# Kernel optimization log

Hardware: AMD Instinct MI355X
Metric: run time of the kernel (lower is better)

## Reference

```python
import jax, jax.numpy as jnp
import numpy as np

B, N, RBF, F = 4, 512, 32, 16
EPS = 1e-7


def _levi_civita():
    e = np.zeros((3, 3, 3), np.float32)
    e[0, 1, 2] = e[1, 2, 0] = e[2, 0, 1] = 1.0
    e[0, 2, 1] = e[2, 1, 0] = e[1, 0, 2] = -1.0
    return jnp.asarray(e)


def setup_inputs() -> dict:
    key = jax.random.key(0)
    ks = jax.random.split(key, 8)
    g = lambda k, s, sc=1.0: jax.random.normal(k, s, dtype=jnp.float32) * sc
    w_sc = RBF ** -0.5
    return dict(
        image=jax.random.uniform(ks[0], (B, N, N, RBF), dtype=jnp.float32),
        vectors=g(ks[1], (B, N, N, 3)),
        feat0=g(ks[2], (B, N, F, 1)),
        feat1=g(ks[3], (B, N, F, 3)),
        W00=g(ks[4], (RBF, F), w_sc), b00=jnp.zeros((F,), jnp.float32),
        W01=g(ks[5], (RBF, F), w_sc), b01=jnp.zeros((F,), jnp.float32),
        W10=g(ks[6], (RBF, F), w_sc), b10=jnp.zeros((F,), jnp.float32),
        W11=g(ks[7], (RBF, F), w_sc), b11=jnp.zeros((F,), jnp.float32),
    )


def _masked(radial, vectors):
    # zero the radial where the pair vector has (near) zero norm (self-pairs)
    keep = jnp.linalg.norm(vectors, axis=-1) >= EPS  # (B,N,N)
    return jnp.where(keep[..., None], radial, jnp.zeros_like(radial))


def reference(image, vectors, feat0, feat1, W00, b00, W01, b01, W10, b10, W11, b11):
    # radial networks: Dense(rbf -> F), one per (input tensor, filter order)
    r00 = image @ W00 + b00                      # (B,N,N,F) RO0 filter for RO0 input
    r01 = _masked(image @ W01 + b01, vectors)    # RO1 filter for RO0 input
    r10 = image @ W10 + b10                      # RO0 filter for RO1 input
    r11 = _masked(image @ W11 + b11, vectors)    # RO1 filter for RO1 input

    f0 = feat0[..., 0]                           # (B,N,F)
    # Note: RO1 filter F1[m,a,b,f,j] = vectors[m,a,b,j] * masked_radial[m,a,b,f];
    # fused into the einsums to avoid materializing (B,N,N,F,3).
    out1 = jnp.einsum('mabf,mbf->maf', r00, f0)[..., None]                 # 0x0->0
    out2 = jnp.einsum('mabi,mabf,mbf->mafi', vectors, r01, f0)             # 1x0->1
    out3 = jnp.einsum('mabf,mbfi->mafi', r10, feat1)                       # 0x1->1
    out4 = jnp.einsum('mabj,mabf,mbfj->maf', vectors, r11, feat1)[..., None]  # 1x1->0
    e = _levi_civita()
    out5 = jnp.einsum('ijk,mabj,mabf,mbfk->mafi', e, vectors, r11, feat1)  # 1x1->1
    return (out1, out2, out3, out4, out5)
```

## Files before the change

kernel.cpp:

```cpp
#include <hip/hip_runtime.h>
#include <hip/hip_bf16.h>


typedef __attribute__((ext_vector_type(8))) short short8;
typedef __attribute__((ext_vector_type(4))) float f32x4;

#define EPS2 1e-14f

static __device__ __forceinline__ short f2bf(float x) {
    __hip_bfloat16 h = __float2bfloat16(x);
    return *reinterpret_cast<short*>(&h);
}

__global__ __launch_bounds__(256, 4) void conv_mfma_vec_kernel(
    const float* __restrict__ image,
    const float* __restrict__ vectors,
    const float* __restrict__ feat0,
    const float* __restrict__ feat1,
    const float* __restrict__ W00, const float* __restrict__ b00,
    const float* __restrict__ W01, const float* __restrict__ b01,
    const float* __restrict__ W10, const float* __restrict__ b10,
    const float* __restrict__ W11, const float* __restrict__ b11,
    float* __restrict__ out)
{
    __shared__ float red[4][16][12];

    const int t    = threadIdx.x;
    const int wave = t >> 6;
    const int lane = t & 63;
    const int f    = lane & 15;
    const int g    = lane >> 4;
    const int ma   = blockIdx.x;
    const int m    = ma >> 9;

    short8 wf0, wf1, wf2, wf3;
    float bias0, bias1, bias2, bias3;
    {
        #pragma unroll
        for (int j = 0; j < 8; ++j) {
            const int k = g * 8 + j;
            wf0[j] = f2bf(W00[k * 16 + f]);
            wf1[j] = f2bf(W01[k * 16 + f]);
            wf2[j] = f2bf(W10[k * 16 + f]);
            wf3[j] = f2bf(W11[k * 16 + f]);
        }
        bias0 = b00[f]; bias1 = b01[f]; bias2 = b10[f]; bias3 = b11[f];
    }

    const float* imgbase = image   + (size_t)ma * (512 * 32);
    const float* vecbase = vectors + (size_t)ma * (512 * 3);
    const float* f0base  = feat0   + (size_t)m  * (512 * 16);
    const float* f1base  = feat1   + (size_t)m  * (512 * 16 * 3);

    float acc1 = 0.f, acc4 = 0.f;
    float acc2x = 0.f, acc2y = 0.f, acc2z = 0.f;
    float acc3x = 0.f, acc3y = 0.f, acc3z = 0.f;
    float acc5x = 0.f, acc5y = 0.f, acc5z = 0.f;

    const int bbase = wave * 128;

#define TAIL(R00, R01, R10, R11, VX, VY, VZ, F0V, U0, U1, U2) { \
    const float vx_ = (VX), vy_ = (VY), vz_ = (VZ); \
    const float n2_ = vx_ * vx_ + vy_ * vy_ + vz_ * vz_; \
    const bool keep_ = n2_ >= EPS2; \
    const float r00_ = (R00); \
    const float r01_ = keep_ ? (R01) : 0.f; \
    const float r10_ = (R10); \
    const float r11_ = keep_ ? (R11) : 0.f; \
    const float f0v_ = (F0V); \
    const float u0_ = (U0), u1_ = (U1), u2_ = (U2); \
    acc1 = fmaf(r00_, f0v_, acc1); \
    const float t01_ = r01_ * f0v_; \
    acc2x = fmaf(t01_, vx_, acc2x); \
    acc2y = fmaf(t01_, vy_, acc2y); \
    acc2z = fmaf(t01_, vz_, acc2z); \
    acc3x = fmaf(r10_, u0_, acc3x); \
    acc3y = fmaf(r10_, u1_, acc3y); \
    acc3z = fmaf(r10_, u2_, acc3z); \
    const float dd_ = fmaf(vx_, u0_, fmaf(vy_, u1_, vz_ * u2_)); \
    acc4 = fmaf(r11_, dd_, acc4); \
    acc5x = fmaf(r11_, vy_ * u2_ - vz_ * u1_, acc5x); \
    acc5y = fmaf(r11_, vz_ * u0_ - vx_ * u2_, acc5y); \
    acc5z = fmaf(r11_, vx_ * u1_ - vy_ * u0_, acc5z); \
}

    for (int tt = 0; tt < 8; ++tt) {
        const int b0 = bbase + tt * 16;

        const float* arow = imgbase + (size_t)(b0 + f) * 32 + g * 8;
        const float4 a0 = *(const float4*)(arow);
        const float4 a1 = *(const float4*)(arow + 4);

        const int bb = b0 + 4 * g;
        const float* vp = vecbase + bb * 3;
        const float4 V0 = *(const float4*)(vp);
        const float4 V1 = *(const float4*)(vp + 4);
        const float4 V2 = *(const float4*)(vp + 8);
        const float* f0p = f0base + bb * 16 + f;
        const float F0a = f0p[0], F0b = f0p[16], F0c = f0p[32], F0d = f0p[48];
        const float* f1p = f1base + (size_t)(bb * 16 + f) * 3;
        const float3 U_0 = *(const float3*)(f1p);
        const float3 U_1 = *(const float3*)(f1p + 48);
        const float3 U_2 = *(const float3*)(f1p + 96);
        const float3 U_3 = *(const float3*)(f1p + 144);

        short8 af;
        af[0] = f2bf(a0.x); af[1] = f2bf(a0.y);
        af[2] = f2bf(a0.z); af[3] = f2bf(a0.w);
        af[4] = f2bf(a1.x); af[5] = f2bf(a1.y);
        af[6] = f2bf(a1.z); af[7] = f2bf(a1.w);

        f32x4 d0 = {bias0, bias0, bias0, bias0};
        f32x4 d1 = {bias1, bias1, bias1, bias1};
        f32x4 d2 = {bias2, bias2, bias2, bias2};
        f32x4 d3 = {bias3, bias3, bias3, bias3};
        d0 = __builtin_amdgcn_mfma_f32_16x16x32_bf16(af, wf0, d0, 0, 0, 0);
        d1 = __builtin_amdgcn_mfma_f32_16x16x32_bf16(af, wf1, d1, 0, 0, 0);
        d2 = __builtin_amdgcn_mfma_f32_16x16x32_bf16(af, wf2, d2, 0, 0, 0);
        d3 = __builtin_amdgcn_mfma_f32_16x16x32_bf16(af, wf3, d3, 0, 0, 0);

        TAIL(d0[0], d1[0], d2[0], d3[0], V0.x, V0.y, V0.z, F0a, U_0.x, U_0.y, U_0.z)
        TAIL(d0[1], d1[1], d2[1], d3[1], V0.w, V1.x, V1.y, F0b, U_1.x, U_1.y, U_1.z)
        TAIL(d0[2], d1[2], d2[2], d3[2], V1.z, V1.w, V2.x, F0c, U_2.x, U_2.y, U_2.z)
        TAIL(d0[3], d1[3], d2[3], d3[3], V2.y, V2.z, V2.w, F0d, U_3.x, U_3.y, U_3.z)
    }
#undef TAIL

    #define WRED(x) x += __shfl_xor(x, 16); x += __shfl_xor(x, 32);
    WRED(acc1)  WRED(acc2x) WRED(acc2y) WRED(acc2z)
    WRED(acc3x) WRED(acc3y) WRED(acc3z) WRED(acc4)
    WRED(acc5x) WRED(acc5y) WRED(acc5z)
    #undef WRED

    if (lane < 16) {
        red[wave][f][0]  = acc1;
        red[wave][f][1]  = acc2x;
        red[wave][f][2]  = acc2y;
        red[wave][f][3]  = acc2z;
        red[wave][f][4]  = acc3x;
        red[wave][f][5]  = acc3y;
        red[wave][f][6]  = acc3z;
        red[wave][f][7]  = acc4;
        red[wave][f][8]  = acc5x;
        red[wave][f][9]  = acc5y;
        red[wave][f][10] = acc5z;
    }
    __syncthreads();

    if (t < 176) {
        const int ff = t / 11;
        const int comp = t % 11;
        float s = red[0][ff][comp] + red[1][ff][comp]
                + red[2][ff][comp] + red[3][ff][comp];

        const size_t base16 = (size_t)ma * 16 + ff;
        const size_t base48 = base16 * 3;
        if (comp == 0)      out[base16] = s;
        else if (comp < 4)  out[32768  + base48 + (comp - 1)] = s;
        else if (comp < 7)  out[131072 + base48 + (comp - 4)] = s;
        else if (comp == 7) out[229376 + base16] = s;
        else                out[262144 + base48 + (comp - 8)] = s;
    }
}

extern "C" void kernel_launch(void* const* d_in, const int* in_sizes, int n_in,
                              void* d_out, int out_size, void* d_ws, size_t ws_size,
                              hipStream_t stream) {
    const float* image   = (const float*)d_in[0];
    const float* vectors = (const float*)d_in[1];
    const float* feat0   = (const float*)d_in[2];
    const float* feat1   = (const float*)d_in[3];
    const float* W00 = (const float*)d_in[4];
    const float* b00 = (const float*)d_in[5];
    const float* W01 = (const float*)d_in[6];
    const float* b01 = (const float*)d_in[7];
    const float* W10 = (const float*)d_in[8];
    const float* b10 = (const float*)d_in[9];
    const float* W11 = (const float*)d_in[10];
    const float* b11 = (const float*)d_in[11];
    float* out = (float*)d_out;

    conv_mfma_vec_kernel<<<4 * 512, 256, 0, stream>>>(
        image, vectors, feat0, feat1,
        W00, b00, W01, b01, W10, b10, W11, b11, out);
}
```

Measured before the change: 226.0 us.

## Double-buffer image and feature tiles in LDS via async global_load_lds

Each wave now stages its image, feat0 and feat1 tiles into a per-wave double buffer in LDS using direct global-to-LDS loads. The next tile is prefetched while the current one is processed, and an XOR swizzle on image rows is meant to avoid bank conflicts. This aims to hide global load latency behind the MFMA and tail arithmetic. In exchange it uses about 48KB of LDS per block, lowers launch bounds occupancy from 4 to 3, and waits on vmcnt(0), which also stalls on the vector loads each iteration.

```diff
diff --git a/kernel.cpp b/kernel.cpp
--- a/kernel.cpp
+++ b/kernel.cpp
@@ -12,7 +12,14 @@
     return *reinterpret_cast<short*>(&h);
 }
 
-__global__ __launch_bounds__(256, 4) void conv_mfma_vec_kernel(
+static __device__ __forceinline__ void gload16(const void* g, void* l) {
+    __builtin_amdgcn_global_load_lds(
+        (const __attribute__((address_space(1))) void*)g,
+        (__attribute__((address_space(3))) void*)l,
+        16, 0, 0);
+}
+
+__global__ __launch_bounds__(256, 3) void conv_mfma_ldspipe_kernel(
     const float* __restrict__ image,
     const float* __restrict__ vectors,
     const float* __restrict__ feat0,
@@ -23,6 +30,7 @@
     const float* __restrict__ W11, const float* __restrict__ b11,
     float* __restrict__ out)
 {
+    __shared__ __align__(16) char smem[4 * 2 * 6144];
     __shared__ float red[4][16][12];
 
     const int t    = threadIdx.x;
@@ -58,6 +66,21 @@
     float acc5x = 0.f, acc5y = 0.f, acc5z = 0.f;
 
     const int bbase = wave * 128;
+    const unsigned wlds = (unsigned)wave * 12288u;
+
+#define STAGE(TT, DST) { \
+    const char* imgT_ = (const char*)(imgbase + (size_t)(bbase + (TT) * 16) * 32); \
+    const char* f0T_  = (const char*)(f0base + (bbase + (TT) * 16) * 16); \
+    const char* f1T_  = (const char*)(f1base + (size_t)(bbase + (TT) * 16) * 48); \
+    { const int i_ = lane;      const int r_ = i_ >> 3, s_ = i_ & 7; \
+      gload16(imgT_ + (((r_ << 3) + (s_ ^ (r_ & 7))) << 4), smem + (DST)); } \
+    { const int i_ = lane + 64; const int r_ = i_ >> 3, s_ = i_ & 7; \
+      gload16(imgT_ + (((r_ << 3) + (s_ ^ (r_ & 7))) << 4), smem + (DST) + 1024); } \
+    gload16(f0T_ + (lane << 4),        smem + (DST) + 2048); \
+    gload16(f1T_ + (lane << 4),        smem + (DST) + 3072); \
+    gload16(f1T_ + (lane << 4) + 1024, smem + (DST) + 4096); \
+    gload16(f1T_ + (lane << 4) + 2048, smem + (DST) + 5120); \
+}
 
 #define TAIL(R00, R01, R10, R11, VX, VY, VZ, F0V, U0, U1, U2) { \
     const float vx_ = (VX), vy_ = (VY), vz_ = (VZ); \
@@ -84,25 +107,46 @@
     acc5z = fmaf(r11_, vx_ * u1_ - vy_ * u0_, acc5z); \
 }
 
+    STAGE(0, wlds)
+
+    #pragma unroll
     for (int tt = 0; tt < 8; ++tt) {
-        const int b0 = bbase + tt * 16;
-
-        const float* arow = imgbase + (size_t)(b0 + f) * 32 + g * 8;
-        const float4 a0 = *(const float4*)(arow);
-        const float4 a1 = *(const float4*)(arow + 4);
-
-        const int bb = b0 + 4 * g;
+        const int cur = tt & 1;
+
+        asm volatile("s_waitcnt vmcnt(0)" ::: "memory");
+        __builtin_amdgcn_sched_barrier(0);
+
+        const char* cb = smem + wlds + (unsigned)cur * 6144u;
+        const float4 a0 = *(const float4*)(cb + f * 128 + (((2 * g)     ^ (f & 7)) << 4));
+        const float4 a1 = *(const float4*)(cb + f * 128 + (((2 * g + 1) ^ (f & 7)) << 4));
+        const float* f0s = (const float*)(cb + 2048);
+        const float F0a = f0s[(4 * g + 0) * 16 + f];
+        const float F0b = f0s[(4 * g + 1) * 16 + f];
+        const float F0c = f0s[(4 * g + 2) * 16 + f];
+        const float F0d = f0s[(4 * g + 3) * 16 + f];
+        const float* f1s = (const float*)(cb + 3072);
+        const float U00 = f1s[(4 * g + 0) * 48 + f * 3 + 0];
+        const float U01 = f1s[(4 * g + 0) * 48 + f * 3 + 1];
+        const float U02 = f1s[(4 * g + 0) * 48 + f * 3 + 2];
+        const float U10 = f1s[(4 * g + 1) * 48 + f * 3 + 0];
+        const float U11 = f1s[(4 * g + 1) * 48 + f * 3 + 1];
+        const float U12 = f1s[(4 * g + 1) * 48 + f * 3 + 2];
+        const float U20 = f1s[(4 * g + 2) * 48 + f * 3 + 0];
+        const float U21 = f1s[(4 * g + 2) * 48 + f * 3 + 1];
+        const float U22 = f1s[(4 * g + 2) * 48 + f * 3 + 2];
+        const float U30 = f1s[(4 * g + 3) * 48 + f * 3 + 0];
+        const float U31 = f1s[(4 * g + 3) * 48 + f * 3 + 1];
+        const float U32 = f1s[(4 * g + 3) * 48 + f * 3 + 2];
+
+        const int bb = bbase + tt * 16 + 4 * g;
         const float* vp = vecbase + bb * 3;
         const float4 V0 = *(const float4*)(vp);
         const float4 V1 = *(const float4*)(vp + 4);
         const float4 V2 = *(const float4*)(vp + 8);
-        const float* f0p = f0base + bb * 16 + f;
-        const float F0a = f0p[0], F0b = f0p[16], F0c = f0p[32], F0d = f0p[48];
-        const float* f1p = f1base + (size_t)(bb * 16 + f) * 3;
-        const float3 U_0 = *(const float3*)(f1p);
-        const float3 U_1 = *(const float3*)(f1p + 48);
-        const float3 U_2 = *(const float3*)(f1p + 96);
-        const float3 U_3 = *(const float3*)(f1p + 144);
+
+        __builtin_amdgcn_sched_barrier(0);
+        if (tt < 7) { STAGE(tt + 1, wlds + (unsigned)(cur ^ 1) * 6144u) }
+        __builtin_amdgcn_sched_barrier(0);
 
         short8 af;
         af[0] = f2bf(a0.x); af[1] = f2bf(a0.y);
@@ -119,12 +163,13 @@
         d2 = __builtin_amdgcn_mfma_f32_16x16x32_bf16(af, wf2, d2, 0, 0, 0);
         d3 = __builtin_amdgcn_mfma_f32_16x16x32_bf16(af, wf3, d3, 0, 0, 0);
 
-        TAIL(d0[0], d1[0], d2[0], d3[0], V0.x, V0.y, V0.z, F0a, U_0.x, U_0.y, U_0.z)
-        TAIL(d0[1], d1[1], d2[1], d3[1], V0.w, V1.x, V1.y, F0b, U_1.x, U_1.y, U_1.z)
-        TAIL(d0[2], d1[2], d2[2], d3[2], V1.z, V1.w, V2.x, F0c, U_2.x, U_2.y, U_2.z)
-        TAIL(d0[3], d1[3], d2[3], d3[3], V2.y, V2.z, V2.w, F0d, U_3.x, U_3.y, U_3.z)
+        TAIL(d0[0], d1[0], d2[0], d3[0], V0.x, V0.y, V0.z, F0a, U00, U01, U02)
+        TAIL(d0[1], d1[1], d2[1], d3[1], V0.w, V1.x, V1.y, F0b, U10, U11, U12)
+        TAIL(d0[2], d1[2], d2[2], d3[2], V1.z, V1.w, V2.x, F0c, U20, U21, U22)
+        TAIL(d0[3], d1[3], d2[3], d3[3], V2.y, V2.z, V2.w, F0d, U30, U31, U32)
     }
 #undef TAIL
+#undef STAGE
 
     #define WRED(x) x += __shfl_xor(x, 16); x += __shfl_xor(x, 32);
     WRED(acc1)  WRED(acc2x) WRED(acc2y) WRED(acc2z)
@@ -180,7 +225,7 @@
     const float* b11 = (const float*)d_in[11];
     float* out = (float*)d_out;
 
-    conv_mfma_vec_kernel<<<4 * 512, 256, 0, stream>>>(
+    conv_mfma_ldspipe_kernel<<<4 * 512, 256, 0, stream>>>(
         image, vectors, feat0, feat1,
         W00, b00, W01, b01, W10, b10, W11, b11, out);
 }
```

Measured after the change: 361.7 us. +60.1%, slower.

## Double-buffer image and feature tiles in LDS via async global-to-LDS loads

Applied to the files above, without the earlier changes.

Each wave now stages its image rows plus feat0 and feat1 slices into a per-wave double buffer in shared memory using global_load_lds. The next tile is prefetched while the current one is consumed. The image tile is stored with an XOR swizzle and a row permutation, so the MFMA output rows map to interleaved b indices, and the vector loads are remapped to match. The aim is to hide global-load latency in a kernel that is bandwidth- and latency-limited. The cost is 48KB of LDS per block, which may lower occupancy, and a block-wide barrier on every iteration.

```diff
diff --git a/kernel.cpp b/kernel.cpp
--- a/kernel.cpp
+++ b/kernel.cpp
@@ -12,7 +12,14 @@
     return *reinterpret_cast<short*>(&h);
 }
 
-__global__ __launch_bounds__(256, 4) void conv_mfma_vec_kernel(
+static __device__ __forceinline__ void gload16(const void* g, void* l) {
+    __builtin_amdgcn_global_load_lds(
+        (const __attribute__((address_space(1))) void*)g,
+        (__attribute__((address_space(3))) void*)l,
+        16, 0, 0);
+}
+
+__global__ __launch_bounds__(256, 4) void conv_mfma_coop_kernel(
     const float* __restrict__ image,
     const float* __restrict__ vectors,
     const float* __restrict__ feat0,
@@ -23,6 +30,7 @@
     const float* __restrict__ W11, const float* __restrict__ b11,
     float* __restrict__ out)
 {
+    __shared__ __align__(16) char smem[4 * 2 * 6144];
     __shared__ float red[4][16][12];
 
     const int t    = threadIdx.x;
@@ -58,6 +66,27 @@
     float acc5x = 0.f, acc5y = 0.f, acc5z = 0.f;
 
     const int bbase = wave * 128;
+    const unsigned wlds = (unsigned)wave * 12288u;
+
+    const int r0 = lane >> 3, s0 = lane & 7;
+    const int sr0 = ((r0 & 3) << 2) + (r0 >> 2);
+    const int isrc0 = sr0 * 128 + ((s0 ^ (r0 & 7)) << 4);
+    const int r1 = r0 + 8;
+    const int sr1 = ((r1 & 3) << 2) + (r1 >> 2);
+    const int isrc1 = sr1 * 128 + ((s0 ^ (r1 & 7)) << 4);
+
+#define STAGE(TT, BUF) { \
+    const char* imgT_ = (const char*)(imgbase + (size_t)(bbase + (TT) * 16) * 32); \
+    const char* f0T_  = (const char*)(f0base + (bbase + (TT) * 16) * 16); \
+    const char* f1T_  = (const char*)(f1base + (size_t)(bbase + (TT) * 16) * 48); \
+    char* db_ = smem + wlds + (BUF) * 6144; \
+    gload16(imgT_ + isrc0, db_); \
+    gload16(imgT_ + isrc1, db_ + 1024); \
+    gload16(f0T_ + (lane << 4), db_ + 2048); \
+    gload16(f1T_ + (lane << 4), db_ + 3072); \
+    gload16(f1T_ + (lane << 4) + 1024, db_ + 4096); \
+    gload16(f1T_ + (lane << 4) + 2048, db_ + 5120); \
+}
 
 #define TAIL(R00, R01, R10, R11, VX, VY, VZ, F0V, U0, U1, U2) { \
     const float vx_ = (VX), vy_ = (VY), vz_ = (VZ); \
@@ -84,25 +113,35 @@
     acc5z = fmaf(r11_, vx_ * u1_ - vy_ * u0_, acc5z); \
 }
 
+    STAGE(0, 0)
+
+    #pragma unroll
     for (int tt = 0; tt < 8; ++tt) {
-        const int b0 = bbase + tt * 16;
-
-        const float* arow = imgbase + (size_t)(b0 + f) * 32 + g * 8;
-        const float4 a0 = *(const float4*)(arow);
-        const float4 a1 = *(const float4*)(arow + 4);
-
-        const int bb = b0 + 4 * g;
-        const float* vp = vecbase + bb * 3;
-        const float4 V0 = *(const float4*)(vp);
-        const float4 V1 = *(const float4*)(vp + 4);
-        const float4 V2 = *(const float4*)(vp + 8);
-        const float* f0p = f0base + bb * 16 + f;
-        const float F0a = f0p[0], F0b = f0p[16], F0c = f0p[32], F0d = f0p[48];
-        const float* f1p = f1base + (size_t)(bb * 16 + f) * 3;
-        const float3 U_0 = *(const float3*)(f1p);
-        const float3 U_1 = *(const float3*)(f1p + 48);
-        const float3 U_2 = *(const float3*)(f1p + 96);
-        const float3 U_3 = *(const float3*)(f1p + 144);
+        __syncthreads();
+
+        if (tt < 7) { STAGE(tt + 1, (tt + 1) & 1) }
+
+        const char* cb = smem + wlds + (unsigned)(tt & 1) * 6144u;
+
+        const float4 a0 = *(const float4*)(cb + f * 128 + (((2 * g)     ^ (f & 7)) << 4));
+        const float4 a1 = *(const float4*)(cb + f * 128 + (((2 * g + 1) ^ (f & 7)) << 4));
+
+        const float* f0s = (const float*)(cb + 2048);
+        const float F0a = f0s[(g     ) * 16 + f];
+        const float F0b = f0s[(g +  4) * 16 + f];
+        const float F0c = f0s[(g +  8) * 16 + f];
+        const float F0d = f0s[(g + 12) * 16 + f];
+        const float* f1s = (const float*)(cb + 3072);
+        const float3 U_0 = *(const float3*)(f1s + (g     ) * 48 + f * 3);
+        const float3 U_1 = *(const float3*)(f1s + (g +  4) * 48 + f * 3);
+        const float3 U_2 = *(const float3*)(f1s + (g +  8) * 48 + f * 3);
+        const float3 U_3 = *(const float3*)(f1s + (g + 12) * 48 + f * 3);
+
+        const float* vp = vecbase + (bbase + tt * 16 + g) * 3;
+        const float3 V_0 = *(const float3*)(vp);
+        const float3 V_1 = *(const float3*)(vp + 12);
+        const float3 V_2 = *(const float3*)(vp + 24);
+        const float3 V_3 = *(const float3*)(vp + 36);
 
         short8 af;
         af[0] = f2bf(a0.x); af[1] = f2bf(a0.y);
@@ -119,12 +158,13 @@
         d2 = __builtin_amdgcn_mfma_f32_16x16x32_bf16(af, wf2, d2, 0, 0, 0);
         d3 = __builtin_amdgcn_mfma_f32_16x16x32_bf16(af, wf3, d3, 0, 0, 0);
 
-        TAIL(d0[0], d1[0], d2[0], d3[0], V0.x, V0.y, V0.z, F0a, U_0.x, U_0.y, U_0.z)
-        TAIL(d0[1], d1[1], d2[1], d3[1], V0.w, V1.x, V1.y, F0b, U_1.x, U_1.y, U_1.z)
-        TAIL(d0[2], d1[2], d2[2], d3[2], V1.z, V1.w, V2.x, F0c, U_2.x, U_2.y, U_2.z)
-        TAIL(d0[3], d1[3], d2[3], d3[3], V2.y, V2.z, V2.w, F0d, U_3.x, U_3.y, U_3.z)
+        TAIL(d0[0], d1[0], d2[0], d3[0], V_0.x, V_0.y, V_0.z, F0a, U_0.x, U_0.y, U_0.z)
+        TAIL(d0[1], d1[1], d2[1], d3[1], V_1.x, V_1.y, V_1.z, F0b, U_1.x, U_1.y, U_1.z)
+        TAIL(d0[2], d1[2], d2[2], d3[2], V_2.x, V_2.y, V_2.z, F0c, U_2.x, U_2.y, U_2.z)
+        TAIL(d0[3], d1[3], d2[3], d3[3], V_3.x, V_3.y, V_3.z, F0d, U_3.x, U_3.y, U_3.z)
     }
 #undef TAIL
+#undef STAGE
 
     #define WRED(x) x += __shfl_xor(x, 16); x += __shfl_xor(x, 32);
     WRED(acc1)  WRED(acc2x) WRED(acc2y) WRED(acc2z)
@@ -180,7 +220,7 @@
     const float* b11 = (const float*)d_in[11];
     float* out = (float*)d_out;
 
-    conv_mfma_vec_kernel<<<4 * 512, 256, 0, stream>>>(
+    conv_mfma_coop_kernel<<<4 * 512, 256, 0, stream>>>(
         image, vectors, feat0, feat1,
         W00, b00, W01, b01, W10, b10, W11, b11, out);
 }
```

Result: slower. 270.0 us (+19.5%).

## Double-buffer image tiles in LDS via async global_load_lds prefetch

Applied to the files above, without the earlier changes.

Image rows are now staged into a per-wave, XOR-swizzled LDS double buffer using global-to-LDS direct loads. The next 16-row tile is prefetched while the current one goes through MFMA and the tail math. This aims to hide global load latency on the image stream, which is the dominant traffic. In exchange it adds a block-wide barrier each iteration and disables unrolling. It also relies on the barrier being enough to complete the async LDS writes, with no explicit vmcnt wait.

```diff
diff --git a/kernel.cpp b/kernel.cpp
--- a/kernel.cpp
+++ b/kernel.cpp
@@ -12,7 +12,14 @@
     return *reinterpret_cast<short*>(&h);
 }
 
-__global__ __launch_bounds__(256, 4) void conv_mfma_vec_kernel(
+static __device__ __forceinline__ void gload16(const void* g, void* l) {
+    __builtin_amdgcn_global_load_lds(
+        (const __attribute__((address_space(1))) void*)g,
+        (__attribute__((address_space(3))) void*)l,
+        16, 0, 0);
+}
+
+__global__ __launch_bounds__(256, 4) void conv_mfma_imgstage_kernel(
     const float* __restrict__ image,
     const float* __restrict__ vectors,
     const float* __restrict__ feat0,
@@ -23,6 +30,7 @@
     const float* __restrict__ W11, const float* __restrict__ b11,
     float* __restrict__ out)
 {
+    __shared__ __align__(16) char smem[4 * 2 * 2048];
     __shared__ float red[4][16][12];
 
     const int t    = threadIdx.x;
@@ -58,6 +66,19 @@
     float acc5x = 0.f, acc5y = 0.f, acc5z = 0.f;
 
     const int bbase = wave * 128;
+    char* wbase = smem + wave * 4096;
+
+    const int r0 = lane >> 3, s0 = lane & 7;
+    const int isrc0 = r0 * 128 + ((s0 ^ (r0 & 7)) << 4);
+    const int a0_off = f * 128 + (((2 * g)     ^ (f & 7)) << 4);
+    const int a1_off = f * 128 + (((2 * g + 1) ^ (f & 7)) << 4);
+
+#define STAGE(TT, BUF) { \
+    const char* imgT_ = (const char*)(imgbase + (size_t)(bbase + (TT) * 16) * 32); \
+    char* db_ = wbase + (BUF) * 2048; \
+    gload16(imgT_ + isrc0,        db_); \
+    gload16(imgT_ + isrc0 + 1024, db_ + 1024); \
+}
 
 #define TAIL(R00, R01, R10, R11, VX, VY, VZ, F0V, U0, U1, U2) { \
     const float vx_ = (VX), vy_ = (VY), vz_ = (VZ); \
@@ -84,14 +105,19 @@
     acc5z = fmaf(r11_, vx_ * u1_ - vy_ * u0_, acc5z); \
 }
 
+    STAGE(0, 0)
+
+    #pragma unroll 1
     for (int tt = 0; tt < 8; ++tt) {
-        const int b0 = bbase + tt * 16;
-
-        const float* arow = imgbase + (size_t)(b0 + f) * 32 + g * 8;
-        const float4 a0 = *(const float4*)(arow);
-        const float4 a1 = *(const float4*)(arow + 4);
-
-        const int bb = b0 + 4 * g;
+        __syncthreads();
+
+        if (tt < 7) { STAGE(tt + 1, (tt + 1) & 1) }
+
+        const char* cb = wbase + (tt & 1) * 2048;
+        const float4 a0 = *(const float4*)(cb + a0_off);
+        const float4 a1 = *(const float4*)(cb + a1_off);
+
+        const int bb = bbase + tt * 16 + 4 * g;
         const float* vp = vecbase + bb * 3;
         const float4 V0 = *(const float4*)(vp);
         const float4 V1 = *(const float4*)(vp + 4);
@@ -125,6 +151,7 @@
         TAIL(d0[3], d1[3], d2[3], d3[3], V2.y, V2.z, V2.w, F0d, U_3.x, U_3.y, U_3.z)
     }
 #undef TAIL
+#undef STAGE
 
     #define WRED(x) x += __shfl_xor(x, 16); x += __shfl_xor(x, 32);
     WRED(acc1)  WRED(acc2x) WRED(acc2y) WRED(acc2z)
@@ -180,7 +207,7 @@
     const float* b11 = (const float*)d_in[11];
     float* out = (float*)d_out;
 
-    conv_mfma_vec_kernel<<<4 * 512, 256, 0, stream>>>(
+    conv_mfma_imgstage_kernel<<<4 * 512, 256, 0, stream>>>(
         image, vectors, feat0, feat1,
         W00, b00, W01, b01, W10, b10, W11, b11, out);
 }
```

Result: no change. 222.4 us (-1.6%).
